# Kernel tuning notes

Measured on AMD Instinct MI355X. Metric: run time of the kernel, lower is better.

Reference implementation:

```python
import jax, jax.numpy as jnp
import numpy as np
from jax import lax

GRID = 16
EPS = 1e-5


def setup_inputs() -> dict:
    key = jax.random.key(0)
    ks = jax.random.split(key, 6)
    B, Cin, H, W = 4, 3, 512, 512
    x = jax.random.normal(ks[0], (B, Cin, H, W), dtype=jnp.float32)
    w1 = jax.random.normal(ks[1], (256, Cin, 3, 3), dtype=jnp.float32) * 0.05
    b1 = jnp.zeros((256,), jnp.float32)
    bn_gamma = jnp.ones((256,), jnp.float32)
    bn_beta = jnp.zeros((256,), jnp.float32)
    bn_mean = jnp.zeros((256,), jnp.float32)
    bn_var = jnp.ones((256,), jnp.float32)
    w2 = jax.random.normal(ks[2], (128, 256), dtype=jnp.float32) * 0.05
    b2 = jnp.zeros((128,), jnp.float32)
    w3 = jax.random.normal(ks[3], (16, 128), dtype=jnp.float32) * 0.05
    b3 = jnp.zeros((16,), jnp.float32)
    return {"x": x, "w1": w1, "b1": b1, "bn_gamma": bn_gamma, "bn_beta": bn_beta,
            "bn_mean": bn_mean, "bn_var": bn_var, "w2": w2, "b2": b2, "w3": w3, "b3": b3}


def reference(x, w1, b1, bn_gamma, bn_beta, bn_mean, bn_var, w2, b2, w3, b3):
    B, _, H, W = x.shape
    # feature extractor: 3x3 conv -> BN (eval, running stats) -> ReLU
    feat = lax.conv_general_dilated(x, w1, (1, 1), 'SAME',
                                    dimension_numbers=('NCHW', 'OIHW', 'NCHW'))
    feat = feat + b1[None, :, None, None]
    inv = bn_gamma * lax.rsqrt(bn_var + EPS)
    feat = jax.nn.relu(feat * inv[None, :, None, None] + (bn_beta - bn_mean * inv)[None, :, None, None])
    # classifier: 1x1 conv -> ReLU -> 1x1 conv
    h = jax.nn.relu(jnp.einsum('bchw,oc->bohw', feat, w2) + b2[None, :, None, None])
    logits = jnp.einsum('bchw,oc->bohw', h, w3) + b3[None, :, None, None]  # [B,C,H,W]
    C = logits.shape[1]
    # grid segments: nearest upsample of grid ids == floor block assignment
    grid_h, grid_w = H // GRID, W // GRID
    S = grid_h * grid_w
    seg_row = (jnp.arange(H) * grid_h) // H
    seg_col = (jnp.arange(W) * grid_w) // W
    seg = (seg_row[:, None] * grid_w + seg_col[None, :]).reshape(-1)  # [H*W]
    # segment mean pooling (single fused scatter-add pass)
    data = logits.reshape(B, C, H * W).transpose(2, 0, 1)  # [HW,B,C]
    sums = jax.ops.segment_sum(data, seg, num_segments=S)  # [S,B,C]
    counts = jax.ops.segment_sum(jnp.ones((H * W,), logits.dtype), seg, num_segments=S)
    pooled = (sums / counts[:, None, None]).transpose(1, 2, 0)  # [B,C,S]
    # F.interpolate([B,C,S,1] -> (H,W), nearest): row h <- floor(h*S/H), col <- 0
    row_idx = (jnp.arange(H) * S) // H
    out = pooled[:, :, row_idx]  # [B,C,H]
    return jnp.broadcast_to(out[..., None], (B, C, H, W))
```

## Files before the change

kernel.cpp:

```cpp
#include <hip/hip_runtime.h>

typedef __attribute__((ext_vector_type(8))) short short8;
typedef __attribute__((ext_vector_type(4))) float f32x4;

#define MFMA(a, b, c) __builtin_amdgcn_mfma_f32_16x16x32_bf16(a, b, c, 0, 0, 0)

__device__ __forceinline__ unsigned short f2bf16(float f) {
    __bf16 h = (__bf16)f;
    return __builtin_bit_cast(unsigned short, h);
}

__device__ __forceinline__ unsigned cvtpk(float lo, float hi) {
    unsigned r;
    asm("v_cvt_pk_bf16_f32 %0, %1, %2" : "=v"(r) : "v"(lo), "v"(hi));
    return r;
}

__global__ void prep_kernel(const float* __restrict__ w1, const float* __restrict__ b1,
                            const float* __restrict__ gamma, const float* __restrict__ beta,
                            const float* __restrict__ mean, const float* __restrict__ var,
                            const float* __restrict__ w2, const float* __restrict__ w3,
                            unsigned short* __restrict__ w1a, unsigned short* __restrict__ w2a,
                            unsigned short* __restrict__ w3a) {
    int idx = blockIdx.x * 256 + threadIdx.x;
    if (idx < 8192) {
        int mt = idx >> 9, r = idx & 511, lane = r >> 3, e = r & 7;
        int o = mt * 16 + (lane & 15);
        int k = ((lane >> 4) << 3) + e;
        float inv = gamma[o] * rsqrtf(var[o] + 1e-5f);
        float v;
        if (k < 27)       v = w1[o * 27 + k] * inv;
        else if (k == 27) v = b1[o] * inv + beta[o] - mean[o] * inv;
        else              v = 0.0f;
        w1a[idx] = f2bf16(v);
    }
    if (idx < 32768) {
        int tile = idx >> 9, r = idx & 511, lane = r >> 3, e = r & 7;
        int kt = tile >> 3, mt = tile & 7;
        int g = lane >> 4;
        int o = mt * 16 + (lane & 15);
        int kphys = kt * 32 + ((e >> 2) << 4) + (g << 2) + (e & 3);
        w2a[idx] = f2bf16(w2[o * 256 + kphys]);
    }
    if (idx < 2048) {
        int kt = idx >> 9, r = idx & 511, lane = r >> 3, e = r & 7;
        int g = lane >> 4;
        int o = lane & 15;
        int kphys = kt * 32 + ((e >> 2) << 4) + (g << 2) + (e & 3);
        w3a[idx] = f2bf16(w3[o * 128 + kphys]);
    }
}

__global__ __launch_bounds__(512, 4)
void fused_block_kernel(const float* __restrict__ x,
                        const unsigned short* __restrict__ w1a,
                        const unsigned short* __restrict__ w2a,
                        const unsigned short* __restrict__ w3a,
                        const float* __restrict__ b2, const float* __restrict__ b3,
                        float* __restrict__ out) {
    __shared__ __align__(16) unsigned short w2s[32768];
    __shared__ __align__(16) unsigned short patch[3 * 18 * 18];
    __shared__ float poolW[8][16];
    __shared__ float poolF[16];

    int tid = threadIdx.x;
    int bid = blockIdx.x;
    int b  = bid >> 9;
    int br = (bid >> 4) & 31;
    int j  = bid & 15;
    int r0 = br * 16;
    int c0 = j * 32;
    int lane = tid & 63;
    int w = tid >> 6;
    int g = lane >> 4;
    int c = lane & 15;

    #pragma unroll
    for (int it = 0; it < 8; it++) {
        int off = it * 4096 + tid * 8;
        *(uint4*)&w2s[off] = *(const uint4*)&w2a[off];
    }

    for (int i = tid; i < 972; i += 512) {
        int ch = i / 324, rr = (i % 324) / 18, cc = i % 18;
        int gr = r0 + rr - 1, gc = c0 + cc - 1;
        float v = 0.0f;
        if ((unsigned)gr < 512u && (unsigned)gc < 512u)
            v = x[((b * 3 + ch) * 512 + gr) * 512 + gc];
        patch[i] = f2bf16(v);
    }
    __syncthreads();

    int offk[8];
    #pragma unroll
    for (int e = 0; e < 8; e++) {
        int k = g * 8 + e;
        int ch = (k * 7282) >> 16;
        int rem = k - ch * 9;
        int dy = (rem * 21846) >> 16;
        int dx = rem - dy * 3;
        int o = ch * 324 + dy * 18 + dx;
        offk[e] = (k < 27) ? o : 0;
    }

    short8 bfr[2];
    #pragma unroll
    for (int nj = 0; nj < 2; nj++) {
        int base = (2 * w + nj) * 18 + c;
        unsigned val[8];
        #pragma unroll
        for (int e = 0; e < 8; e++)
            val[e] = patch[base + offk[e]];
        if (g == 3) {
            val[3] = 0x3F80u;
            val[4] = val[5] = val[6] = val[7] = 0u;
        }
        union { unsigned u[4]; short8 s; } uu;
        #pragma unroll
        for (int q = 0; q < 4; q++)
            uu.u[q] = val[2 * q] | (val[2 * q + 1] << 16);
        bfr[nj] = uu.s;
    }

    f32x4 acc2[8][2];
    #pragma unroll
    for (int m = 0; m < 8; m++) {
        acc2[m][0] = (f32x4){0.f, 0.f, 0.f, 0.f};
        acc2[m][1] = (f32x4){0.f, 0.f, 0.f, 0.f};
    }
    const f32x4 zero = {0.f, 0.f, 0.f, 0.f};

    #pragma unroll
    for (int kt = 0; kt < 8; kt++) {
        short8 w1f0 = *(const short8*)&w1a[(kt * 2 + 0) * 512 + lane * 8];
        short8 w1f1 = *(const short8*)&w1a[(kt * 2 + 1) * 512 + lane * 8];
        short8 b2f[2];
        #pragma unroll
        for (int nj = 0; nj < 2; nj++) {
            f32x4 a0 = MFMA(w1f0, bfr[nj], zero);
            f32x4 a1 = MFMA(w1f1, bfr[nj], zero);
            union { unsigned u[4]; short8 s; } uu;
            uu.u[0] = cvtpk(fmaxf(a0[0], 0.f), fmaxf(a0[1], 0.f));
            uu.u[1] = cvtpk(fmaxf(a0[2], 0.f), fmaxf(a0[3], 0.f));
            uu.u[2] = cvtpk(fmaxf(a1[0], 0.f), fmaxf(a1[1], 0.f));
            uu.u[3] = cvtpk(fmaxf(a1[2], 0.f), fmaxf(a1[3], 0.f));
            b2f[nj] = uu.s;
        }
        #pragma unroll
        for (int m = 0; m < 8; m++) {
            short8 w2f = *(const short8*)&w2s[(kt * 8 + m) * 512 + lane * 8];
            acc2[m][0] = MFMA(w2f, b2f[0], acc2[m][0]);
            acc2[m][1] = MFMA(w2f, b2f[1], acc2[m][1]);
        }
    }

    f32x4 accP[2] = {zero, zero};
    #pragma unroll
    for (int kt = 0; kt < 4; kt++) {
        short8 w3f = *(const short8*)&w3a[kt * 512 + lane * 8];
        f32x4 bA = *(const f32x4*)&b2[(2 * kt + 0) * 16 + g * 4];
        f32x4 bB = *(const f32x4*)&b2[(2 * kt + 1) * 16 + g * 4];
        #pragma unroll
        for (int nj = 0; nj < 2; nj++) {
            f32x4 a0 = acc2[2 * kt + 0][nj];
            f32x4 a1 = acc2[2 * kt + 1][nj];
            union { unsigned u[4]; short8 s; } uu;
            uu.u[0] = cvtpk(fmaxf(a0[0] + bA[0], 0.f), fmaxf(a0[1] + bA[1], 0.f));
            uu.u[1] = cvtpk(fmaxf(a0[2] + bA[2], 0.f), fmaxf(a0[3] + bA[3], 0.f));
            uu.u[2] = cvtpk(fmaxf(a1[0] + bB[0], 0.f), fmaxf(a1[1] + bB[1], 0.f));
            uu.u[3] = cvtpk(fmaxf(a1[2] + bB[2], 0.f), fmaxf(a1[3] + bB[3], 0.f));
            accP[nj] = MFMA(w3f, uu.s, accP[nj]);
        }
    }

    float v0 = accP[0][0] + accP[1][0];
    float v1 = accP[0][1] + accP[1][1];
    float v2 = accP[0][2] + accP[1][2];
    float v3 = accP[0][3] + accP[1][3];
    #pragma unroll
    for (int off = 1; off < 16; off <<= 1) {
        v0 += __shfl_xor(v0, off);
        v1 += __shfl_xor(v1, off);
        v2 += __shfl_xor(v2, off);
        v3 += __shfl_xor(v3, off);
    }
    if (c == 0) {
        poolW[w][g * 4 + 0] = v0;
        poolW[w][g * 4 + 1] = v1;
        poolW[w][g * 4 + 2] = v2;
        poolW[w][g * 4 + 3] = v3;
    }
    __syncthreads();
    if (tid < 16) {
        float s = 0.f;
        #pragma unroll
        for (int ww = 0; ww < 8; ww++) s += poolW[ww][tid];
        poolF[tid] = s * (1.0f / 256.0f) + b3[tid];
    }
    __syncthreads();

    int h = r0 + j;
    int cc = tid >> 5;
    float pv = poolF[cc];
    float4 vv = {pv, pv, pv, pv};
    float4* rowp = (float4*)(out + (size_t)(((b * 16 + cc) * 512 + h)) * 512);
    int base = tid & 31;
    #pragma unroll
    for (int ii = 0; ii < 4; ii++)
        rowp[ii * 32 + base] = vv;
}

extern "C" void kernel_launch(void* const* d_in, const int* in_sizes, int n_in,
                              void* d_out, int out_size, void* d_ws, size_t ws_size,
                              hipStream_t stream) {
    const float* x     = (const float*)d_in[0];
    const float* w1    = (const float*)d_in[1];
    const float* b1    = (const float*)d_in[2];
    const float* gamma = (const float*)d_in[3];
    const float* beta  = (const float*)d_in[4];
    const float* mean  = (const float*)d_in[5];
    const float* var   = (const float*)d_in[6];
    const float* w2    = (const float*)d_in[7];
    const float* b2    = (const float*)d_in[8];
    const float* w3    = (const float*)d_in[9];
    const float* b3    = (const float*)d_in[10];
    float* out = (float*)d_out;

    unsigned short* w1a = (unsigned short*)d_ws;
    unsigned short* w2a = w1a + 8192;
    unsigned short* w3a = w2a + 32768;

    prep_kernel<<<128, 256, 0, stream>>>(w1, b1, gamma, beta, mean, var, w2, w3,
                                         w1a, w2a, w3a);
    fused_block_kernel<<<2048, 512, 0, stream>>>(x, w1a, w2a, w3a, b2, b3, out);
}
```

Baseline: 57.57 us.

## Software-pipeline conv and w2 fragment loads in fused MFMA loop

Restructures the main K loop into a double-buffered pipeline. The next stage's conv MFMA outputs, the w1 fragments and the w2 LDS fragments are prefetched while the current w2 MFMAs run, to hide LDS and global load latency. The launch bound is relaxed from 4 to 2 blocks per CU to allow more registers for the extra buffers. The inline-asm packed bf16 convert is also replaced by scalar conversions. The added register pressure, lower occupancy target and possibly costlier conversion may offset the gain.

After: 59.56 us. 3.5% more time.

```diff
diff --git a/kernel.cpp b/kernel.cpp
--- a/kernel.cpp
+++ b/kernel.cpp
@@ -10,10 +10,8 @@
     return __builtin_bit_cast(unsigned short, h);
 }
 
-__device__ __forceinline__ unsigned cvtpk(float lo, float hi) {
-    unsigned r;
-    asm("v_cvt_pk_bf16_f32 %0, %1, %2" : "=v"(r) : "v"(lo), "v"(hi));
-    return r;
+__device__ __forceinline__ unsigned pk2(float lo, float hi) {
+    return (unsigned)f2bf16(lo) | ((unsigned)f2bf16(hi) << 16);
 }
 
 __global__ void prep_kernel(const float* __restrict__ w1, const float* __restrict__ b1,
@@ -51,7 +49,7 @@
     }
 }
 
-__global__ __launch_bounds__(512, 4)
+__global__ __launch_bounds__(512, 2)
 void fused_block_kernel(const float* __restrict__ x,
                         const unsigned short* __restrict__ w1a,
                         const unsigned short* __restrict__ w2a,
@@ -130,27 +128,61 @@
     }
     const f32x4 zero = {0.f, 0.f, 0.f, 0.f};
 
+    short8 w1f0, w1f1;
+    short8 w2c[8], w2n[8];
+    short8 b2c[2], b2n[2];
+
+    w1f0 = *(const short8*)&w1a[0 * 512 + lane * 8];
+    w1f1 = *(const short8*)&w1a[1 * 512 + lane * 8];
+    #pragma unroll
+    for (int nj = 0; nj < 2; nj++) {
+        f32x4 a0 = MFMA(w1f0, bfr[nj], zero);
+        f32x4 a1 = MFMA(w1f1, bfr[nj], zero);
+        union { unsigned u[4]; short8 s; } uu;
+        uu.u[0] = pk2(fmaxf(a0[0], 0.f), fmaxf(a0[1], 0.f));
+        uu.u[1] = pk2(fmaxf(a0[2], 0.f), fmaxf(a0[3], 0.f));
+        uu.u[2] = pk2(fmaxf(a1[0], 0.f), fmaxf(a1[1], 0.f));
+        uu.u[3] = pk2(fmaxf(a1[2], 0.f), fmaxf(a1[3], 0.f));
+        b2c[nj] = uu.s;
+    }
+    w1f0 = *(const short8*)&w1a[2 * 512 + lane * 8];
+    w1f1 = *(const short8*)&w1a[3 * 512 + lane * 8];
+    #pragma unroll
+    for (int m = 0; m < 8; m++)
+        w2c[m] = *(const short8*)&w2s[m * 512 + lane * 8];
+
     #pragma unroll
     for (int kt = 0; kt < 8; kt++) {
-        short8 w1f0 = *(const short8*)&w1a[(kt * 2 + 0) * 512 + lane * 8];
-        short8 w1f1 = *(const short8*)&w1a[(kt * 2 + 1) * 512 + lane * 8];
-        short8 b2f[2];
-        #pragma unroll
-        for (int nj = 0; nj < 2; nj++) {
-            f32x4 a0 = MFMA(w1f0, bfr[nj], zero);
-            f32x4 a1 = MFMA(w1f1, bfr[nj], zero);
-            union { unsigned u[4]; short8 s; } uu;
-            uu.u[0] = cvtpk(fmaxf(a0[0], 0.f), fmaxf(a0[1], 0.f));
-            uu.u[1] = cvtpk(fmaxf(a0[2], 0.f), fmaxf(a0[3], 0.f));
-            uu.u[2] = cvtpk(fmaxf(a1[0], 0.f), fmaxf(a1[1], 0.f));
-            uu.u[3] = cvtpk(fmaxf(a1[2], 0.f), fmaxf(a1[3], 0.f));
-            b2f[nj] = uu.s;
+        if (kt < 7) {
+            #pragma unroll
+            for (int nj = 0; nj < 2; nj++) {
+                f32x4 a0 = MFMA(w1f0, bfr[nj], zero);
+                f32x4 a1 = MFMA(w1f1, bfr[nj], zero);
+                union { unsigned u[4]; short8 s; } uu;
+                uu.u[0] = pk2(fmaxf(a0[0], 0.f), fmaxf(a0[1], 0.f));
+                uu.u[1] = pk2(fmaxf(a0[2], 0.f), fmaxf(a0[3], 0.f));
+                uu.u[2] = pk2(fmaxf(a1[0], 0.f), fmaxf(a1[1], 0.f));
+                uu.u[3] = pk2(fmaxf(a1[2], 0.f), fmaxf(a1[3], 0.f));
+                b2n[nj] = uu.s;
+            }
+            if (kt < 6) {
+                w1f0 = *(const short8*)&w1a[(kt * 2 + 4) * 512 + lane * 8];
+                w1f1 = *(const short8*)&w1a[(kt * 2 + 5) * 512 + lane * 8];
+            }
+            #pragma unroll
+            for (int m = 0; m < 8; m++)
+                w2n[m] = *(const short8*)&w2s[((kt + 1) * 8 + m) * 512 + lane * 8];
         }
         #pragma unroll
         for (int m = 0; m < 8; m++) {
-            short8 w2f = *(const short8*)&w2s[(kt * 8 + m) * 512 + lane * 8];
-            acc2[m][0] = MFMA(w2f, b2f[0], acc2[m][0]);
-            acc2[m][1] = MFMA(w2f, b2f[1], acc2[m][1]);
+            acc2[m][0] = MFMA(w2c[m], b2c[0], acc2[m][0]);
+            acc2[m][1] = MFMA(w2c[m], b2c[1], acc2[m][1]);
+        }
+        if (kt < 7) {
+            #pragma unroll
+            for (int m = 0; m < 8; m++) w2c[m] = w2n[m];
+            b2c[0] = b2n[0];
+            b2c[1] = b2n[1];
         }
     }
 
@@ -165,10 +197,10 @@
             f32x4 a0 = acc2[2 * kt + 0][nj];
             f32x4 a1 = acc2[2 * kt + 1][nj];
             union { unsigned u[4]; short8 s; } uu;
-            uu.u[0] = cvtpk(fmaxf(a0[0] + bA[0], 0.f), fmaxf(a0[1] + bA[1], 0.f));
-            uu.u[1] = cvtpk(fmaxf(a0[2] + bA[2], 0.f), fmaxf(a0[3] + bA[3], 0.f));
-            uu.u[2] = cvtpk(fmaxf(a1[0] + bB[0], 0.f), fmaxf(a1[1] + bB[1], 0.f));
-            uu.u[3] = cvtpk(fmaxf(a1[2] + bB[2], 0.f), fmaxf(a1[3] + bB[3], 0.f));
+            uu.u[0] = pk2(fmaxf(a0[0] + bA[0], 0.f), fmaxf(a0[1] + bA[1], 0.f));
+            uu.u[1] = pk2(fmaxf(a0[2] + bA[2], 0.f), fmaxf(a0[3] + bA[3], 0.f));
+            uu.u[2] = pk2(fmaxf(a1[0] + bB[0], 0.f), fmaxf(a1[1] + bB[1], 0.f));
+            uu.u[3] = pk2(fmaxf(a1[2] + bB[2], 0.f), fmaxf(a1[3] + bB[3], 0.f));
             accP[nj] = MFMA(w3f, uu.s, accP[nj]);
         }
     }
```
